# Kernel tuning notes

Hardware: AMD Instinct MI355X
Metric: run time of the kernel (lower is better)

The kernel has to match this reference:

```python
import math
import jax, jax.numpy as jnp
import numpy as np

K = 16  # self.k from init


def knn(x, x2, k):
    # x: [B, d, P], x2: [B, d, S] -> nearest-neighbor indices [B, k, S]
    # (indices into P, per query column of x2). Matches torch knn: topk of
    # negative squared distance along dim=-2.
    x = jax.lax.stop_gradient(x)
    x2 = jax.lax.stop_gradient(x2)
    inner = -2.0 * jnp.einsum('bdp,bds->bps', x, x2)            # [B, P, S]
    xx = jnp.sum(x * x, axis=1)[:, :, None]                      # [B, P, 1]
    xx2 = jnp.sum(x2 * x2, axis=1)[:, None, :]                   # [B, 1, S]
    pd = -xx - inner - xx2                                       # [B, P, S]
    # top-k over the P axis -> move P to last axis for lax.top_k
    _, idx = jax.lax.top_k(jnp.transpose(pd, (0, 2, 1)), k)     # [B, S, k]
    return jnp.transpose(idx, (0, 2, 1))                         # [B, k, S]


def gather_neighbour(X, idx):
    # X: [B, C, P], idx: [B, n, p] -> [B, p, n, C]
    g = jax.vmap(lambda Xb, ib: Xb[:, ib])(X, idx)               # [B, C, n, p]
    return jnp.transpose(g, (0, 3, 2, 1))


def _forward(x, s_num):
    B, C, P = x.shape
    assert s_num <= P
    length = math.ceil(math.sqrt(s_num))                         # 64
    L2 = length * length                                         # == s_num (perfect square)
    mesh = jnp.arange(length, dtype=x.dtype) / length
    m01 = jnp.tile(mesh[None, :], (length, 1)).reshape(1, 1, L2)
    m02 = jnp.tile(mesh[:, None], (1, length)).reshape(1, 1, L2)
    mesh2 = jnp.concatenate([m01, m02], axis=1)                  # [1, 2, L2]
    mesh2 = jnp.broadcast_to(mesh2, (B, 2, L2))

    point_x = x[:, :2, :]                                        # [B, 2, P]
    min_x = jnp.min(point_x, axis=2, keepdims=True)
    max_x = jnp.max(point_x, axis=2, keepdims=True)
    point_sample = mesh2 * (max_x - min_x) + min_x               # [B, 2, L2]

    idx1 = knn(point_x, point_sample, 1)                         # [B, 1, L2]
    sel = gather_neighbour(x, idx1)                              # [B, L2, 1, C]
    select_point = jnp.transpose(sel[:, :, 0, :], (0, 2, 1))     # [B, C, L2]

    idx2 = knn(x[:, :3, :], select_point[:, :3, :], K)           # [B, K, s_num]
    feature = gather_neighbour(x, idx2)                          # [B, s_num, K, C]
    return jnp.transpose(feature, (0, 3, 1, 2))                  # [B, C, s_num, K]


def setup_inputs() -> dict:
    key = jax.random.key(0)
    x = jax.random.normal(key, (8, 5, 16384), dtype=jnp.float32)
    return {"x": x, "s_num": 4096}


def reference(x, s_num):
    return _forward(x, s_num)
```

## Files before the change

kernel.cpp:

```cpp
#include <hip/hip_runtime.h>

#define P 16384
#define S 4096
#define NB 8
#define CAP 16

typedef unsigned long long u64;
typedef unsigned int u32;

#define OPAQUE(x) __asm__("" : "+v"(x))

__device__ __forceinline__ u32 pd_to_dk(float pd) {
  pd = pd + 0.0f;
  u32 b = __float_as_uint(pd);
  u32 s = (u32)((int)b >> 31);
  return b ^ (~(s | 0x80000000u));
}
__device__ __forceinline__ float dk_to_pd(u32 d) {
  u32 pb = (d & 0x80000000u) ? d : (d ^ 0x7FFFFFFFu);
  return __uint_as_float(pb);
}
__device__ __forceinline__ float prev2(float v) {
  u32 b = __float_as_uint(v);
  if ((b & 0x7F800000u) == 0x7F800000u) return v;
  if (v > 0.0f) b -= 2;
  else if (v < 0.0f) b += 2;
  else return -1e-30f;
  return __uint_as_float(b);
}

__device__ __forceinline__ void insert16(u64 (&L)[16], u64 key) {
#pragma unroll
  for (int j = 15; j >= 1; --j) {
    u64 a = (L[j - 1] > key) ? L[j - 1] : key;
    L[j] = (L[j] > key) ? a : L[j];
  }
  L[0] = (L[0] > key) ? key : L[0];
}

__global__ void kminmax(const float* __restrict__ x, float* __restrict__ mm) {
  int b = blockIdx.x;
  int tid = threadIdx.x;
  const float* x0 = x + (size_t)b * 5 * P;
  const float* x1 = x0 + P;
  float mn0 = __builtin_inff(), mx0 = -__builtin_inff();
  float mn1 = __builtin_inff(), mx1 = -__builtin_inff();
  for (int i = tid; i < P; i += 256) {
    float a = x0[i];
    mn0 = fminf(mn0, a); mx0 = fmaxf(mx0, a);
    float c = x1[i];
    mn1 = fminf(mn1, c); mx1 = fmaxf(mx1, c);
  }
  __shared__ float s0[256], s1[256], s2[256], s3[256];
  s0[tid] = mn0; s1[tid] = mx0; s2[tid] = mn1; s3[tid] = mx1;
  __syncthreads();
  for (int off = 128; off > 0; off >>= 1) {
    if (tid < off) {
      s0[tid] = fminf(s0[tid], s0[tid + off]);
      s1[tid] = fmaxf(s1[tid], s1[tid + off]);
      s2[tid] = fminf(s2[tid], s2[tid + off]);
      s3[tid] = fmaxf(s3[tid], s3[tid + off]);
    }
    __syncthreads();
  }
  if (tid == 0) {
    mm[b * 4 + 0] = s0[0];
    mm[b * 4 + 1] = s1[0];
    mm[b * 4 + 2] = s2[0];
    mm[b * 4 + 3] = s3[0];
  }
}

__global__ void kprep(const float* __restrict__ x, float* __restrict__ xx2d,
                      float* __restrict__ xx3d) {
#pragma clang fp contract(off)
  int gid = blockIdx.x * 256 + threadIdx.x;
  int b = gid >> 14;
  int i = gid & (P - 1);
  const float* xs = x + (size_t)b * 5 * P;
  float x0 = xs[i], x1 = xs[P + i], x2 = xs[2 * P + i];
  float t0 = x0 * x0; OPAQUE(t0);
  float t1 = x1 * x1; OPAQUE(t1);
  float t2 = x2 * x2; OPAQUE(t2);
  float s2 = t0 + t1;
  xx2d[gid] = s2;
  xx3d[gid] = s2 + t2;
}

__global__ __launch_bounds__(256) void kidx1(const float* __restrict__ x,
                                             const float* __restrict__ mm,
                                             const float* __restrict__ xx2d,
                                             u64* __restrict__ bests1) {
#pragma clang fp contract(off)
  int blk = blockIdx.x;
  int b = blk >> 8;
  int sgrp = (blk >> 2) & 63;
  int qtr = blk & 3;
  int w = threadIdx.x >> 6, l = threadIdx.x & 63;
  const float* xs = x + (size_t)b * 5 * P;
  const float* ys = xs + P;
  float mn0 = mm[b * 4 + 0], mx0 = mm[b * 4 + 1];
  float mn1 = mm[b * 4 + 2], mx1 = mm[b * 4 + 3];
  float m0 = (float)l * (1.0f / 64.0f);
  float m1 = (float)sgrp * (1.0f / 64.0f);
  float d0 = mx0 - mn0, d1 = mx1 - mn1;
  float p0 = m0 * d0; OPAQUE(p0);
  float q0 = p0 + mn0;
  float p1 = m1 * d1; OPAQUE(p1);
  float q1 = p1 + mn1;
  float sq0 = q0 * q0; OPAQUE(sq0);
  float sq1 = q1 * q1; OPAQUE(sq1);
  float qq = sq0 + sq1;

  int base = qtr * 4096 + w * 1024;
  const float4* xs4 = (const float4*)(xs + base);
  const float4* ys4 = (const float4*)(ys + base);
  const float4* ws4 = (const float4*)(xx2d + b * P + base);
  float best_pd = -__builtin_inff();
  u32 best_idx = 0;
  for (int j = 0; j < 256; ++j) {
    float4 cx = xs4[j];
    float4 cy = ys4[j];
    float4 cw = ws4[j];
    float cxa[4] = {cx.x, cx.y, cx.z, cx.w};
    float cya[4] = {cy.x, cy.y, cy.z, cy.w};
    float cwa[4] = {cw.x, cw.y, cw.z, cw.w};
#pragma unroll
    for (int t = 0; t < 4; ++t) {
      float ip = __builtin_fmaf(cya[t], q1, cxa[t] * q0);
      float a  = __builtin_fmaf(2.0f, ip, -cwa[t]);
      float pd = a - qq;
      bool bt = pd > best_pd;
      best_pd  = bt ? pd : best_pd;
      best_idx = bt ? (u32)(base + (j << 2) + t) : best_idx;
    }
  }
  u64 key = ((u64)pd_to_dk(best_pd) << 32) | best_idx;
  __shared__ u64 kb[4][64];
  kb[w][l] = key;
  __syncthreads();
  if (threadIdx.x < 64) {
    u64 m = kb[0][l];
    u64 t1 = kb[1][l]; m = (t1 < m) ? t1 : m;
    u64 t2 = kb[2][l]; m = (t2 < m) ? t2 : m;
    u64 t3 = kb[3][l]; m = (t3 < m) ? t3 : m;
    bests1[((size_t)((b * 64 + sgrp) * 4 + qtr) << 6) + l] = m;
  }
}

__global__ void kq(const float* __restrict__ x, const u64* __restrict__ bests1,
                   float* __restrict__ qx, float* __restrict__ qy,
                   float* __restrict__ qz) {
  int qi = blockIdx.x * 256 + threadIdx.x;
  int b = qi >> 12;
  int s = qi & 4095;
  int sgrp = s >> 6, l = s & 63;
  size_t o = ((size_t)((b * 64 + sgrp) * 4) << 6) + l;
  u64 m = bests1[o];
  u64 t;
  t = bests1[o + 64];  m = (t < m) ? t : m;
  t = bests1[o + 128]; m = (t < m) ? t : m;
  t = bests1[o + 192]; m = (t < m) ? t : m;
  u32 idx = (u32)m;
  const float* xs = x + (size_t)b * 5 * P;
  qx[qi] = xs[idx];
  qy[qi] = xs[P + idx];
  qz[qi] = xs[2 * P + idx];
}

__global__ __launch_bounds__(512) void kidx2(const float* __restrict__ x,
                                             const float* __restrict__ xx3d,
                                             const float* __restrict__ qx,
                                             const float* __restrict__ qy,
                                             const float* __restrict__ qz,
                                             float* __restrict__ out) {
#pragma clang fp contract(off)
  __shared__ u64 buf[512][CAP + 1];
  __shared__ u64 mgf[64][17];
  int b = blockIdx.x >> 6, sgrp = blockIdx.x & 63;
  int w = threadIdx.x >> 6, l = threadIdx.x & 63;
  int s = (sgrp << 6) + l;
  int qi = (b << 12) + s;
  float q0 = qx[qi], q1 = qy[qi], q2 = qz[qi];
  float sq0 = q0 * q0; OPAQUE(sq0);
  float sq1 = q1 * q1; OPAQUE(sq1);
  float sq2 = q2 * q2; OPAQUE(sq2);
  float qq = (sq0 + sq1) + sq2;
  const float* xs = x + (size_t)b * 5 * P;
  const float* ys = xs + P;
  const float* zs = xs + 2 * P;
  int base = w * 2048;
  const float4* xs4 = (const float4*)(xs + base);
  const float4* ys4 = (const float4*)(ys + base);
  const float4* zs4 = (const float4*)(zs + base);
  const float4* ws4 = (const float4*)(xx3d + b * P + base);

  u64 L[16];
#pragma unroll
  for (int k = 0; k < 16; ++k) L[k] = 0xFF800000FFFFFFFFull;
  float thrA = -__builtin_inff();
  int cnt = 0;
  u64* bufp = buf[threadIdx.x];

  auto drain = [&]() {
    while (__any(cnt > 0)) {
      if (cnt > 0) {
        --cnt;
        u64 e = bufp[cnt];
        float pd = __uint_as_float((u32)(e >> 32)) - qq;
        u64 key = ((u64)pd_to_dk(pd) << 32) | (u32)e;
        if (key < L[15]) insert16(L, key);
      }
    }
    float tp = dk_to_pd((u32)(L[15] >> 32));
    thrA = prev2(tp + qq);
  };

  for (int j = 0; j < 512; ++j) {
    float4 cx = xs4[j];
    float4 cy = ys4[j];
    float4 cz = zs4[j];
    float4 cw = ws4[j];
    float cxa[4] = {cx.x, cx.y, cx.z, cx.w};
    float cya[4] = {cy.x, cy.y, cy.z, cy.w};
    float cza[4] = {cz.x, cz.y, cz.z, cz.w};
    float cwa[4] = {cw.x, cw.y, cw.z, cw.w};
#pragma unroll
    for (int t = 0; t < 4; ++t) {
      float ip = __builtin_fmaf(cza[t], q2,
                                __builtin_fmaf(cya[t], q1, cxa[t] * q0));
      float a  = __builtin_fmaf(2.0f, ip, -cwa[t]);
      if (a >= thrA) {
        bufp[cnt] = ((u64)__float_as_uint(a) << 32) | (u32)(base + (j << 2) + t);
        ++cnt;
      }
    }
    if (__any(cnt >= CAP - 4)) drain();
  }
  drain();

#pragma unroll
  for (int k = 0; k < 16; ++k) bufp[k] = L[k];
  __syncthreads();

  if (w == 0) {
    int p0 = 0, p1 = 0, p2 = 0, p3 = 0, p4 = 0, p5 = 0, p6 = 0, p7 = 0;
    u64 h0 = buf[l][0],        h1 = buf[64 + l][0];
    u64 h2 = buf[128 + l][0],  h3 = buf[192 + l][0];
    u64 h4 = buf[256 + l][0],  h5 = buf[320 + l][0];
    u64 h6 = buf[384 + l][0],  h7 = buf[448 + l][0];
#define ADV(i) { ++p##i; h##i = (p##i < 16) ? buf[i * 64 + l][p##i] : ~0ULL; }
    for (int k = 0; k < 16; ++k) {
      u64 m01 = (h0 < h1) ? h0 : h1;
      u64 m23 = (h2 < h3) ? h2 : h3;
      u64 m45 = (h4 < h5) ? h4 : h5;
      u64 m67 = (h6 < h7) ? h6 : h7;
      u64 ma = (m01 < m23) ? m01 : m23;
      u64 mb = (m45 < m67) ? m45 : m67;
      u64 m = (ma < mb) ? ma : mb;
      mgf[l][k] = m;
      if      (m == h0) ADV(0)
      else if (m == h1) ADV(1)
      else if (m == h2) ADV(2)
      else if (m == h3) ADV(3)
      else if (m == h4) ADV(4)
      else if (m == h5) ADV(5)
      else if (m == h6) ADV(6)
      else              ADV(7)
    }
#undef ADV
  }
  __syncthreads();

  int qrow = threadIdx.x >> 3;
  int g = threadIdx.x & 7;
  int sOut = (sgrp << 6) + qrow;
  u32 i0 = (u32)mgf[qrow][g * 2 + 0];
  u32 i1 = (u32)mgf[qrow][g * 2 + 1];
#pragma unroll
  for (int c = 0; c < 5; ++c) {
    const float* xc = x + (size_t)(b * 5 + c) * P;
    float2 v;
    v.x = xc[i0]; v.y = xc[i1];
    float* op = out + (((size_t)(b * 5 + c) * S + sOut) << 4) + (g << 1);
    *(float2*)op = v;
  }
}

extern "C" void kernel_launch(void* const* d_in, const int* in_sizes, int n_in,
                              void* d_out, int out_size, void* d_ws, size_t ws_size,
                              hipStream_t stream) {
  const float* x = (const float*)d_in[0];
  float* out = (float*)d_out;
  char* ws = (char*)d_ws;
  float* mm    = (float*)ws;
  float* xx2d  = (float*)(ws + 1024);
  float* xx3d  = (float*)(ws + 1024 + 524288);
  u64*   bests1= (u64*)  (ws + 1024 + 2 * 524288);
  float* qx    = (float*)(ws + 1024 + 2 * 524288 + 1048576);
  float* qy    = qx + NB * S;
  float* qz    = qy + NB * S;

  kminmax<<<NB, 256, 0, stream>>>(x, mm);
  kprep<<<NB * P / 256, 256, 0, stream>>>(x, xx2d, xx3d);
  kidx1<<<NB * 256, 256, 0, stream>>>(x, mm, xx2d, bests1);
  kq<<<NB * S / 256, 256, 0, stream>>>(x, bests1, qx, qy, qz);
  kidx2<<<NB * 64, 512, 0, stream>>>(x, xx3d, qx, qy, qz, out);
}
```

Measured before the change: 621.5 us.

## Pack point coords into float4 AoS and split kNN scans across more blocks

```diff
diff --git a/kernel.cpp b/kernel.cpp
--- a/kernel.cpp
+++ b/kernel.cpp
@@ -3,7 +3,7 @@
 #define P 16384
 #define S 4096
 #define NB 8
-#define CAP 16
+#define CAP 8
 
 typedef unsigned long long u64;
 typedef unsigned int u32;
@@ -36,6 +36,15 @@
     L[j] = (L[j] > key) ? a : L[j];
   }
   L[0] = (L[0] > key) ? key : L[0];
+}
+
+__device__ __forceinline__ u64 key3(const float4* __restrict__ pk3b, u32 idx,
+                                    float q0, float q1, float q2, float qq) {
+  float4 v = pk3b[idx];
+  float ip = __builtin_fmaf(v.z, q2, __builtin_fmaf(v.y, q1, v.x * q0));
+  float a  = __builtin_fmaf(2.0f, ip, -v.w);
+  float pd = a - qq;
+  return ((u64)pd_to_dk(pd) << 32) | idx;
 }
 
 __global__ void kminmax(const float* __restrict__ x, float* __restrict__ mm) {
@@ -71,8 +80,8 @@
   }
 }
 
-__global__ void kprep(const float* __restrict__ x, float* __restrict__ xx2d,
-                      float* __restrict__ xx3d) {
+__global__ void kprep(const float* __restrict__ x, float4* __restrict__ pk2,
+                      float4* __restrict__ pk3) {
 #pragma clang fp contract(off)
   int gid = blockIdx.x * 256 + threadIdx.x;
   int b = gid >> 14;
@@ -83,22 +92,19 @@
   float t1 = x1 * x1; OPAQUE(t1);
   float t2 = x2 * x2; OPAQUE(t2);
   float s2 = t0 + t1;
-  xx2d[gid] = s2;
-  xx3d[gid] = s2 + t2;
-}
-
-__global__ __launch_bounds__(256) void kidx1(const float* __restrict__ x,
+  pk2[gid] = make_float4(x0, x1, s2, 0.0f);
+  pk3[gid] = make_float4(x0, x1, x2, s2 + t2);
+}
+
+__global__ __launch_bounds__(256) void kidx1(const float4* __restrict__ pk2,
                                              const float* __restrict__ mm,
-                                             const float* __restrict__ xx2d,
                                              u64* __restrict__ bests1) {
 #pragma clang fp contract(off)
   int blk = blockIdx.x;
-  int b = blk >> 8;
-  int sgrp = (blk >> 2) & 63;
-  int qtr = blk & 3;
+  int b = blk >> 9;
+  int sgrp = (blk >> 3) & 63;
+  int eighth = blk & 7;
   int w = threadIdx.x >> 6, l = threadIdx.x & 63;
-  const float* xs = x + (size_t)b * 5 * P;
-  const float* ys = xs + P;
   float mn0 = mm[b * 4 + 0], mx0 = mm[b * 4 + 1];
   float mn1 = mm[b * 4 + 2], mx1 = mm[b * 4 + 3];
   float m0 = (float)l * (1.0f / 64.0f);
@@ -112,23 +118,16 @@
   float sq1 = q1 * q1; OPAQUE(sq1);
   float qq = sq0 + sq1;
 
-  int base = qtr * 4096 + w * 1024;
-  const float4* xs4 = (const float4*)(xs + base);
-  const float4* ys4 = (const float4*)(ys + base);
-  const float4* ws4 = (const float4*)(xx2d + b * P + base);
+  int base = eighth * 2048 + w * 512;
+  const float4* pc = pk2 + (size_t)b * P + base;
   float best_pd = -__builtin_inff();
   u32 best_idx = 0;
-  for (int j = 0; j < 256; ++j) {
-    float4 cx = xs4[j];
-    float4 cy = ys4[j];
-    float4 cw = ws4[j];
-    float cxa[4] = {cx.x, cx.y, cx.z, cx.w};
-    float cya[4] = {cy.x, cy.y, cy.z, cy.w};
-    float cwa[4] = {cw.x, cw.y, cw.z, cw.w};
+  for (int j = 0; j < 128; ++j) {
 #pragma unroll
     for (int t = 0; t < 4; ++t) {
-      float ip = __builtin_fmaf(cya[t], q1, cxa[t] * q0);
-      float a  = __builtin_fmaf(2.0f, ip, -cwa[t]);
+      float4 v = pc[(j << 2) + t];
+      float ip = __builtin_fmaf(v.y, q1, v.x * q0);
+      float a  = __builtin_fmaf(2.0f, ip, -v.z);
       float pd = a - qq;
       bool bt = pd > best_pd;
       best_pd  = bt ? pd : best_pd;
@@ -144,7 +143,7 @@
     u64 t1 = kb[1][l]; m = (t1 < m) ? t1 : m;
     u64 t2 = kb[2][l]; m = (t2 < m) ? t2 : m;
     u64 t3 = kb[3][l]; m = (t3 < m) ? t3 : m;
-    bests1[((size_t)((b * 64 + sgrp) * 4 + qtr) << 6) + l] = m;
+    bests1[((size_t)((b * 64 + sgrp) * 8 + eighth) << 6) + l] = m;
   }
 }
 
@@ -155,12 +154,13 @@
   int b = qi >> 12;
   int s = qi & 4095;
   int sgrp = s >> 6, l = s & 63;
-  size_t o = ((size_t)((b * 64 + sgrp) * 4) << 6) + l;
+  size_t o = ((size_t)((b * 64 + sgrp) * 8) << 6) + l;
   u64 m = bests1[o];
-  u64 t;
-  t = bests1[o + 64];  m = (t < m) ? t : m;
-  t = bests1[o + 128]; m = (t < m) ? t : m;
-  t = bests1[o + 192]; m = (t < m) ? t : m;
+#pragma unroll
+  for (int i = 1; i < 8; ++i) {
+    u64 t = bests1[o + (size_t)i * 64];
+    m = (t < m) ? t : m;
+  }
   u32 idx = (u32)m;
   const float* xs = x + (size_t)b * 5 * P;
   qx[qi] = xs[idx];
@@ -168,39 +168,35 @@
   qz[qi] = xs[2 * P + idx];
 }
 
-__global__ __launch_bounds__(512) void kidx2(const float* __restrict__ x,
-                                             const float* __restrict__ xx3d,
-                                             const float* __restrict__ qx,
-                                             const float* __restrict__ qy,
-                                             const float* __restrict__ qz,
-                                             float* __restrict__ out) {
+__global__ __launch_bounds__(256, 6) void kidx2(const float4* __restrict__ pk3,
+                                                const float* __restrict__ qx,
+                                                const float* __restrict__ qy,
+                                                const float* __restrict__ qz,
+                                                u32* __restrict__ partial) {
 #pragma clang fp contract(off)
-  __shared__ u64 buf[512][CAP + 1];
-  __shared__ u64 mgf[64][17];
-  int b = blockIdx.x >> 6, sgrp = blockIdx.x & 63;
+  __shared__ u64 buf[256 * (CAP + 1)];
+  u32* stage = (u32*)buf;
+  int blk = blockIdx.x;
+  int b = blk >> 7;
+  int rest = blk & 127;
+  int sgrp = rest >> 1, half = rest & 1;
   int w = threadIdx.x >> 6, l = threadIdx.x & 63;
-  int s = (sgrp << 6) + l;
-  int qi = (b << 12) + s;
+  int qi = (b << 12) + (sgrp << 6) + l;
   float q0 = qx[qi], q1 = qy[qi], q2 = qz[qi];
   float sq0 = q0 * q0; OPAQUE(sq0);
   float sq1 = q1 * q1; OPAQUE(sq1);
   float sq2 = q2 * q2; OPAQUE(sq2);
   float qq = (sq0 + sq1) + sq2;
-  const float* xs = x + (size_t)b * 5 * P;
-  const float* ys = xs + P;
-  const float* zs = xs + 2 * P;
-  int base = w * 2048;
-  const float4* xs4 = (const float4*)(xs + base);
-  const float4* ys4 = (const float4*)(ys + base);
-  const float4* zs4 = (const float4*)(zs + base);
-  const float4* ws4 = (const float4*)(xx3d + b * P + base);
+  const float4* pk3b = pk3 + (size_t)b * P;
+  int base = half * 8192 + w * 2048;
+  const float4* pc = pk3b + base;
 
   u64 L[16];
 #pragma unroll
   for (int k = 0; k < 16; ++k) L[k] = 0xFF800000FFFFFFFFull;
   float thrA = -__builtin_inff();
   int cnt = 0;
-  u64* bufp = buf[threadIdx.x];
+  u64* bufp = buf + threadIdx.x * (CAP + 1);
 
   auto drain = [&]() {
     while (__any(cnt > 0)) {
@@ -217,19 +213,11 @@
   };
 
   for (int j = 0; j < 512; ++j) {
-    float4 cx = xs4[j];
-    float4 cy = ys4[j];
-    float4 cz = zs4[j];
-    float4 cw = ws4[j];
-    float cxa[4] = {cx.x, cx.y, cx.z, cx.w};
-    float cya[4] = {cy.x, cy.y, cy.z, cy.w};
-    float cza[4] = {cz.x, cz.y, cz.z, cz.w};
-    float cwa[4] = {cw.x, cw.y, cw.z, cw.w};
 #pragma unroll
     for (int t = 0; t < 4; ++t) {
-      float ip = __builtin_fmaf(cza[t], q2,
-                                __builtin_fmaf(cya[t], q1, cxa[t] * q0));
-      float a  = __builtin_fmaf(2.0f, ip, -cwa[t]);
+      float4 v = pc[(j << 2) + t];
+      float ip = __builtin_fmaf(v.z, q2, __builtin_fmaf(v.y, q1, v.x * q0));
+      float a  = __builtin_fmaf(2.0f, ip, -v.w);
       if (a >= thrA) {
         bufp[cnt] = ((u64)__float_as_uint(a) << 32) | (u32)(base + (j << 2) + t);
         ++cnt;
@@ -239,51 +227,97 @@
   }
   drain();
 
-#pragma unroll
-  for (int k = 0; k < 16; ++k) bufp[k] = L[k];
-  __syncthreads();
-
-  if (w == 0) {
-    int p0 = 0, p1 = 0, p2 = 0, p3 = 0, p4 = 0, p5 = 0, p6 = 0, p7 = 0;
-    u64 h0 = buf[l][0],        h1 = buf[64 + l][0];
-    u64 h2 = buf[128 + l][0],  h3 = buf[192 + l][0];
-    u64 h4 = buf[256 + l][0],  h5 = buf[320 + l][0];
-    u64 h6 = buf[384 + l][0],  h7 = buf[448 + l][0];
-#define ADV(i) { ++p##i; h##i = (p##i < 16) ? buf[i * 64 + l][p##i] : ~0ULL; }
+  __syncthreads();
+#pragma unroll
+  for (int k = 0; k < 16; ++k) stage[(w << 10) + (l << 4) + k] = (u32)L[k];
+  __syncthreads();
+
+  if ((w & 1) == 0) {
+    const u32* sa = stage + (w << 10) + (l << 4);
+    const u32* sb = stage + ((w + 1) << 10) + (l << 4);
+    int pa = 0, pb = 0;
+    u32 ia = sa[0]; u64 ka = key3(pk3b, ia, q0, q1, q2, qq);
+    u32 ib = sb[0]; u64 kb2 = key3(pk3b, ib, q0, q1, q2, qq);
+    u32* outp = partial + ((((size_t)qi * 2 + half) * 2 + (w >> 1)) << 4);
+    for (int k = 0; k < 16; ++k) {
+      bool ta = ka < kb2;
+      outp[k] = ta ? ia : ib;
+      if (ta) {
+        ++pa;
+        if (pa < 16) { ia = sa[pa]; ka = key3(pk3b, ia, q0, q1, q2, qq); }
+        else ka = ~0ULL;
+      } else {
+        ++pb;
+        if (pb < 16) { ib = sb[pb]; kb2 = key3(pk3b, ib, q0, q1, q2, qq); }
+        else kb2 = ~0ULL;
+      }
+    }
+  }
+}
+
+__global__ __launch_bounds__(256) void km(const float* __restrict__ x,
+                                          const float4* __restrict__ pk3,
+                                          const float* __restrict__ qx,
+                                          const float* __restrict__ qy,
+                                          const float* __restrict__ qz,
+                                          const u32* __restrict__ partial,
+                                          float* __restrict__ out) {
+#pragma clang fp contract(off)
+  __shared__ u32 mg[256][16];
+  int tid = threadIdx.x;
+  int qi0 = blockIdx.x * 256;
+  {
+    int qi = qi0 + tid;
+    int b = qi >> 12;
+    float q0 = qx[qi], q1 = qy[qi], q2 = qz[qi];
+    float sq0 = q0 * q0; OPAQUE(sq0);
+    float sq1 = q1 * q1; OPAQUE(sq1);
+    float sq2 = q2 * q2; OPAQUE(sq2);
+    float qq = (sq0 + sq1) + sq2;
+    const float4* pk3b = pk3 + (size_t)b * P;
+    const u32* lp = partial + ((size_t)qi << 6);
+    int p0 = 0, p1 = 0, p2 = 0, p3 = 0;
+    u32 i0 = lp[0],  i1 = lp[16], i2 = lp[32], i3 = lp[48];
+    u64 h0 = key3(pk3b, i0, q0, q1, q2, qq);
+    u64 h1 = key3(pk3b, i1, q0, q1, q2, qq);
+    u64 h2 = key3(pk3b, i2, q0, q1, q2, qq);
+    u64 h3 = key3(pk3b, i3, q0, q1, q2, qq);
+#define ADVK(n, off) { ++p##n; \
+    if (p##n < 16) { i##n = lp[(off) + p##n]; \
+      h##n = key3(pk3b, i##n, q0, q1, q2, qq); } else h##n = ~0ULL; }
     for (int k = 0; k < 16; ++k) {
       u64 m01 = (h0 < h1) ? h0 : h1;
       u64 m23 = (h2 < h3) ? h2 : h3;
-      u64 m45 = (h4 < h5) ? h4 : h5;
-      u64 m67 = (h6 < h7) ? h6 : h7;
-      u64 ma = (m01 < m23) ? m01 : m23;
-      u64 mb = (m45 < m67) ? m45 : m67;
-      u64 m = (ma < mb) ? ma : mb;
-      mgf[l][k] = m;
-      if      (m == h0) ADV(0)
-      else if (m == h1) ADV(1)
-      else if (m == h2) ADV(2)
-      else if (m == h3) ADV(3)
-      else if (m == h4) ADV(4)
-      else if (m == h5) ADV(5)
-      else if (m == h6) ADV(6)
-      else              ADV(7)
-    }
-#undef ADV
-  }
-  __syncthreads();
-
-  int qrow = threadIdx.x >> 3;
-  int g = threadIdx.x & 7;
-  int sOut = (sgrp << 6) + qrow;
-  u32 i0 = (u32)mgf[qrow][g * 2 + 0];
-  u32 i1 = (u32)mgf[qrow][g * 2 + 1];
-#pragma unroll
-  for (int c = 0; c < 5; ++c) {
-    const float* xc = x + (size_t)(b * 5 + c) * P;
-    float2 v;
-    v.x = xc[i0]; v.y = xc[i1];
-    float* op = out + (((size_t)(b * 5 + c) * S + sOut) << 4) + (g << 1);
-    *(float2*)op = v;
+      u64 m = (m01 < m23) ? m01 : m23;
+      mg[tid][k] = (u32)((m == h0) ? i0 : (m == h1) ? i1 : (m == h2) ? i2 : i3);
+      if      (m == h0) ADVK(0, 0)
+      else if (m == h1) ADVK(1, 16)
+      else if (m == h2) ADVK(2, 32)
+      else              ADVK(3, 48)
+    }
+#undef ADVK
+  }
+  __syncthreads();
+
+#pragma unroll
+  for (int pass = 0; pass < 4; ++pass) {
+    int lq = pass * 64 + (tid >> 2);
+    int g = tid & 3;
+    int qi = qi0 + lq;
+    int b = qi >> 12;
+    int s = qi & 4095;
+    u32 j0 = mg[lq][g * 4 + 0];
+    u32 j1 = mg[lq][g * 4 + 1];
+    u32 j2 = mg[lq][g * 4 + 2];
+    u32 j3 = mg[lq][g * 4 + 3];
+#pragma unroll
+    for (int c = 0; c < 5; ++c) {
+      const float* xc = x + (size_t)(b * 5 + c) * P;
+      float4 v;
+      v.x = xc[j0]; v.y = xc[j1]; v.z = xc[j2]; v.w = xc[j3];
+      float* op = out + (((size_t)(b * 5 + c) * S + s) << 4) + (g << 2);
+      *(float4*)op = v;
+    }
   }
 }
 
@@ -293,17 +327,20 @@
   const float* x = (const float*)d_in[0];
   float* out = (float*)d_out;
   char* ws = (char*)d_ws;
-  float* mm    = (float*)ws;
-  float* xx2d  = (float*)(ws + 1024);
-  float* xx3d  = (float*)(ws + 1024 + 524288);
-  u64*   bests1= (u64*)  (ws + 1024 + 2 * 524288);
-  float* qx    = (float*)(ws + 1024 + 2 * 524288 + 1048576);
-  float* qy    = qx + NB * S;
-  float* qz    = qy + NB * S;
+  size_t off = 0;
+  float*  mm     = (float*)(ws + off);  off += 1024;
+  float4* pk2    = (float4*)(ws + off); off += (size_t)NB * P * 16;
+  float4* pk3    = (float4*)(ws + off); off += (size_t)NB * P * 16;
+  u64*    bests1 = (u64*)(ws + off);    off += (size_t)NB * 64 * 8 * 64 * 8;
+  float*  qx     = (float*)(ws + off);  off += (size_t)NB * S * 4;
+  float*  qy     = (float*)(ws + off);  off += (size_t)NB * S * 4;
+  float*  qz     = (float*)(ws + off);  off += (size_t)NB * S * 4;
+  u32*    partial= (u32*)(ws + off);    off += (size_t)NB * S * 4 * 16 * 4;
 
   kminmax<<<NB, 256, 0, stream>>>(x, mm);
-  kprep<<<NB * P / 256, 256, 0, stream>>>(x, xx2d, xx3d);
-  kidx1<<<NB * 256, 256, 0, stream>>>(x, mm, xx2d, bests1);
+  kprep<<<NB * P / 256, 256, 0, stream>>>(x, pk2, pk3);
+  kidx1<<<NB * 64 * 8, 256, 0, stream>>>(pk2, mm, bests1);
   kq<<<NB * S / 256, 256, 0, stream>>>(x, bests1, qx, qy, qz);
-  kidx2<<<NB * 64, 512, 0, stream>>>(x, xx3d, qx, qy, qz, out);
-}
+  kidx2<<<NB * 64 * 2, 256, 0, stream>>>(pk3, qx, qy, qz, partial);
+  km<<<NB * S / 256, 256, 0, stream>>>(x, pk3, qx, qy, qz, partial, out);
+}
```

After: 867.8 us. +39.6%, slower.

## Split kNN top-16 into value-only threshold pass and index-recovery second pass

Applied to the files above, without the earlier changes.

```diff
diff --git a/kernel.cpp b/kernel.cpp
--- a/kernel.cpp
+++ b/kernel.cpp
@@ -3,7 +3,6 @@
 #define P 16384
 #define S 4096
 #define NB 8
-#define CAP 16
 
 typedef unsigned long long u64;
 typedef unsigned int u32;
@@ -29,10 +28,10 @@
   return __uint_as_float(b);
 }
 
-__device__ __forceinline__ void insert16(u64 (&L)[16], u64 key) {
+__device__ __forceinline__ void insert16u32(u32 (&L)[16], u32 key) {
 #pragma unroll
   for (int j = 15; j >= 1; --j) {
-    u64 a = (L[j - 1] > key) ? L[j - 1] : key;
+    u32 a = (L[j - 1] > key) ? L[j - 1] : key;
     L[j] = (L[j] > key) ? a : L[j];
   }
   L[0] = (L[0] > key) ? key : L[0];
@@ -175,12 +174,12 @@
                                              const float* __restrict__ qz,
                                              float* __restrict__ out) {
 #pragma clang fp contract(off)
-  __shared__ u64 buf[512][CAP + 1];
+  __shared__ u64 smem[512 * 17];
   __shared__ u64 mgf[64][17];
+  const int tid = threadIdx.x;
   int b = blockIdx.x >> 6, sgrp = blockIdx.x & 63;
-  int w = threadIdx.x >> 6, l = threadIdx.x & 63;
-  int s = (sgrp << 6) + l;
-  int qi = (b << 12) + s;
+  int w = tid >> 6, l = tid & 63;
+  int qi = (b << 12) + (sgrp << 6) + l;
   float q0 = qx[qi], q1 = qy[qi], q2 = qz[qi];
   float sq0 = q0 * q0; OPAQUE(sq0);
   float sq1 = q1 * q1; OPAQUE(sq1);
@@ -195,24 +194,24 @@
   const float4* zs4 = (const float4*)(zs + base);
   const float4* ws4 = (const float4*)(xx3d + b * P + base);
 
-  u64 L[16];
-#pragma unroll
-  for (int k = 0; k < 16; ++k) L[k] = 0xFF800000FFFFFFFFull;
+  u32 L[16];
+#pragma unroll
+  for (int k = 0; k < 16; ++k) L[k] = 0xFF800000u;
   float thrA = -__builtin_inff();
   int cnt = 0;
-  u64* bufp = buf[threadIdx.x];
-
-  auto drain = [&]() {
+  u32* arow = (u32*)smem + tid * 13;
+
+  auto drainA = [&]() {
     while (__any(cnt > 0)) {
       if (cnt > 0) {
         --cnt;
-        u64 e = bufp[cnt];
-        float pd = __uint_as_float((u32)(e >> 32)) - qq;
-        u64 key = ((u64)pd_to_dk(pd) << 32) | (u32)e;
-        if (key < L[15]) insert16(L, key);
+        float av = __uint_as_float(arow[cnt]);
+        float pd = av - qq;
+        u32 dk = pd_to_dk(pd);
+        if (dk < L[15]) insert16u32(L, dk);
       }
     }
-    float tp = dk_to_pd((u32)(L[15] >> 32));
+    float tp = dk_to_pd(L[15]);
     thrA = prev2(tp + qq);
   };
 
@@ -230,26 +229,82 @@
       float ip = __builtin_fmaf(cza[t], q2,
                                 __builtin_fmaf(cya[t], q1, cxa[t] * q0));
       float a  = __builtin_fmaf(2.0f, ip, -cwa[t]);
-      if (a >= thrA) {
-        bufp[cnt] = ((u64)__float_as_uint(a) << 32) | (u32)(base + (j << 2) + t);
-        ++cnt;
+      if (a >= thrA) { arow[cnt] = __float_as_uint(a); ++cnt; }
+    }
+    if (__any(cnt >= 8)) drainA();
+  }
+  drainA();
+
+  u32 T = L[15];
+  int c_lt = 0;
+#pragma unroll
+  for (int k = 0; k < 15; ++k) c_lt += (L[k] < T) ? 1 : 0;
+  int need = 16 - c_lt;
+  float T_pd = dk_to_pd(T);
+
+  __syncthreads();
+
+  u64* srow = smem + (size_t)tid * 17;
+  int pc2 = 0, eqc = 0;
+  for (int j = 0; j < 512; ++j) {
+    float4 cx = xs4[j];
+    float4 cy = ys4[j];
+    float4 cz = zs4[j];
+    float4 cw = ws4[j];
+    float cxa[4] = {cx.x, cx.y, cx.z, cx.w};
+    float cya[4] = {cy.x, cy.y, cy.z, cy.w};
+    float cza[4] = {cz.x, cz.y, cz.z, cz.w};
+    float cwa[4] = {cw.x, cw.y, cw.z, cw.w};
+#pragma unroll
+    for (int t = 0; t < 4; ++t) {
+      float ip = __builtin_fmaf(cza[t], q2,
+                                __builtin_fmaf(cya[t], q1, cxa[t] * q0));
+      float a  = __builtin_fmaf(2.0f, ip, -cwa[t]);
+      float pd = a - qq;
+      bool lt = pd > T_pd;
+      bool eq = (pd == T_pd) && (eqc < need);
+      if ((lt || eq) && pc2 < 16) {
+        u32 dk = pd_to_dk(pd);
+        srow[pc2] = ((u64)dk << 32) | (u32)(base + (j << 2) + t);
+        ++pc2;
+        eqc += eq ? 1 : 0;
       }
     }
-    if (__any(cnt >= CAP - 4)) drain();
-  }
-  drain();
-
-#pragma unroll
-  for (int k = 0; k < 16; ++k) bufp[k] = L[k];
+  }
+
+  u64 K[16];
+#pragma unroll
+  for (int k = 0; k < 16; ++k) K[k] = srow[k];
+#pragma unroll
+  for (int p = 1; p < 16; p <<= 1) {
+#pragma unroll
+    for (int k = p; k >= 1; k >>= 1) {
+#pragma unroll
+      for (int j = k & (p - 1); j + k < 16; j += 2 * k) {
+#pragma unroll
+        for (int i = 0; i < k; ++i) {
+          int aa = i + j, bb = i + j + k;
+          if (bb < 16 && (aa / (2 * p)) == (bb / (2 * p))) {
+            u64 xa = K[aa], xb = K[bb];
+            bool g = xa > xb;
+            K[aa] = g ? xb : xa;
+            K[bb] = g ? xa : xb;
+          }
+        }
+      }
+    }
+  }
+#pragma unroll
+  for (int k = 0; k < 16; ++k) srow[k] = K[k];
   __syncthreads();
 
   if (w == 0) {
     int p0 = 0, p1 = 0, p2 = 0, p3 = 0, p4 = 0, p5 = 0, p6 = 0, p7 = 0;
-    u64 h0 = buf[l][0],        h1 = buf[64 + l][0];
-    u64 h2 = buf[128 + l][0],  h3 = buf[192 + l][0];
-    u64 h4 = buf[256 + l][0],  h5 = buf[320 + l][0];
-    u64 h6 = buf[384 + l][0],  h7 = buf[448 + l][0];
-#define ADV(i) { ++p##i; h##i = (p##i < 16) ? buf[i * 64 + l][p##i] : ~0ULL; }
+    u64 h0 = smem[(size_t)(0 * 64 + l) * 17], h1 = smem[(size_t)(1 * 64 + l) * 17];
+    u64 h2 = smem[(size_t)(2 * 64 + l) * 17], h3 = smem[(size_t)(3 * 64 + l) * 17];
+    u64 h4 = smem[(size_t)(4 * 64 + l) * 17], h5 = smem[(size_t)(5 * 64 + l) * 17];
+    u64 h6 = smem[(size_t)(6 * 64 + l) * 17], h7 = smem[(size_t)(7 * 64 + l) * 17];
+#define ADV(i) { ++p##i; h##i = (p##i < 16) ? smem[(size_t)(i * 64 + l) * 17 + p##i] : ~0ULL; }
     for (int k = 0; k < 16; ++k) {
       u64 m01 = (h0 < h1) ? h0 : h1;
       u64 m23 = (h2 < h3) ? h2 : h3;
@@ -272,8 +327,8 @@
   }
   __syncthreads();
 
-  int qrow = threadIdx.x >> 3;
-  int g = threadIdx.x & 7;
+  int qrow = tid >> 3;
+  int g = tid & 7;
   int sOut = (sgrp << 6) + qrow;
   u32 i0 = (u32)mgf[qrow][g * 2 + 0];
   u32 i1 = (u32)mgf[qrow][g * 2 + 1];
```

Measured after the change: 782.2 us. 1.26x slower.

## Pack candidate coordinates and norms into float4 AoS and software-pipeline the scan loops

Applied to the files above, without the earlier changes.

```diff
diff --git a/kernel.cpp b/kernel.cpp
--- a/kernel.cpp
+++ b/kernel.cpp
@@ -71,8 +71,8 @@
   }
 }
 
-__global__ void kprep(const float* __restrict__ x, float* __restrict__ xx2d,
-                      float* __restrict__ xx3d) {
+__global__ void kprep(const float* __restrict__ x, float4* __restrict__ pk2,
+                      float4* __restrict__ pk3) {
 #pragma clang fp contract(off)
   int gid = blockIdx.x * 256 + threadIdx.x;
   int b = gid >> 14;
@@ -83,13 +83,12 @@
   float t1 = x1 * x1; OPAQUE(t1);
   float t2 = x2 * x2; OPAQUE(t2);
   float s2 = t0 + t1;
-  xx2d[gid] = s2;
-  xx3d[gid] = s2 + t2;
-}
-
-__global__ __launch_bounds__(256) void kidx1(const float* __restrict__ x,
+  pk2[gid] = make_float4(x0, x1, s2, 0.0f);
+  pk3[gid] = make_float4(x0, x1, x2, s2 + t2);
+}
+
+__global__ __launch_bounds__(256) void kidx1(const float4* __restrict__ pk2,
                                              const float* __restrict__ mm,
-                                             const float* __restrict__ xx2d,
                                              u64* __restrict__ bests1) {
 #pragma clang fp contract(off)
   int blk = blockIdx.x;
@@ -97,8 +96,6 @@
   int sgrp = (blk >> 2) & 63;
   int qtr = blk & 3;
   int w = threadIdx.x >> 6, l = threadIdx.x & 63;
-  const float* xs = x + (size_t)b * 5 * P;
-  const float* ys = xs + P;
   float mn0 = mm[b * 4 + 0], mx0 = mm[b * 4 + 1];
   float mn1 = mm[b * 4 + 2], mx1 = mm[b * 4 + 3];
   float m0 = (float)l * (1.0f / 64.0f);
@@ -113,28 +110,34 @@
   float qq = sq0 + sq1;
 
   int base = qtr * 4096 + w * 1024;
-  const float4* xs4 = (const float4*)(xs + base);
-  const float4* ys4 = (const float4*)(ys + base);
-  const float4* ws4 = (const float4*)(xx2d + b * P + base);
+  const float4* pc = pk2 + (size_t)b * P + base;
   float best_pd = -__builtin_inff();
   u32 best_idx = 0;
-  for (int j = 0; j < 256; ++j) {
-    float4 cx = xs4[j];
-    float4 cy = ys4[j];
-    float4 cw = ws4[j];
-    float cxa[4] = {cx.x, cx.y, cx.z, cx.w};
-    float cya[4] = {cy.x, cy.y, cy.z, cy.w};
-    float cwa[4] = {cw.x, cw.y, cw.z, cw.w};
-#pragma unroll
-    for (int t = 0; t < 4; ++t) {
-      float ip = __builtin_fmaf(cya[t], q1, cxa[t] * q0);
-      float a  = __builtin_fmaf(2.0f, ip, -cwa[t]);
-      float pd = a - qq;
-      bool bt = pd > best_pd;
-      best_pd  = bt ? pd : best_pd;
-      best_idx = bt ? (u32)(base + (j << 2) + t) : best_idx;
-    }
-  }
+
+  float4 B0[4], B1[4], B2[4], B3[4];
+#define LD1(buf, jv) { const float4* _p = pc + ((jv) << 2); \
+  buf[0] = _p[0]; buf[1] = _p[1]; buf[2] = _p[2]; buf[3] = _p[3]; }
+#define EV1(buf, jv) { _Pragma("unroll") \
+  for (int t = 0; t < 4; ++t) { float4 v = buf[t]; \
+    float ip = __builtin_fmaf(v.y, q1, v.x * q0); \
+    float a  = __builtin_fmaf(2.0f, ip, -v.z); \
+    float pd = a - qq; \
+    bool bt = pd > best_pd; \
+    best_pd  = bt ? pd : best_pd; \
+    best_idx = bt ? (u32)(base + ((jv) << 2) + t) : best_idx; } }
+
+  LD1(B0, 0) LD1(B1, 1) LD1(B2, 2) LD1(B3, 3)
+  for (int jj = 0; jj < 64; ++jj) {
+    int j0 = jj << 2;
+    int nb = (jj < 63) ? ((jj + 1) << 2) : j0;
+    EV1(B0, j0)     LD1(B0, nb)
+    EV1(B1, j0 + 1) LD1(B1, nb + 1)
+    EV1(B2, j0 + 2) LD1(B2, nb + 2)
+    EV1(B3, j0 + 3) LD1(B3, nb + 3)
+  }
+#undef LD1
+#undef EV1
+
   u64 key = ((u64)pd_to_dk(best_pd) << 32) | best_idx;
   __shared__ u64 kb[4][64];
   kb[w][l] = key;
@@ -168,8 +171,8 @@
   qz[qi] = xs[2 * P + idx];
 }
 
-__global__ __launch_bounds__(512) void kidx2(const float* __restrict__ x,
-                                             const float* __restrict__ xx3d,
+__global__ __launch_bounds__(512) void kidx2(const float4* __restrict__ pk3,
+                                             const float* __restrict__ x,
                                              const float* __restrict__ qx,
                                              const float* __restrict__ qy,
                                              const float* __restrict__ qz,
@@ -179,21 +182,14 @@
   __shared__ u64 mgf[64][17];
   int b = blockIdx.x >> 6, sgrp = blockIdx.x & 63;
   int w = threadIdx.x >> 6, l = threadIdx.x & 63;
-  int s = (sgrp << 6) + l;
-  int qi = (b << 12) + s;
+  int qi = (b << 12) + (sgrp << 6) + l;
   float q0 = qx[qi], q1 = qy[qi], q2 = qz[qi];
   float sq0 = q0 * q0; OPAQUE(sq0);
   float sq1 = q1 * q1; OPAQUE(sq1);
   float sq2 = q2 * q2; OPAQUE(sq2);
   float qq = (sq0 + sq1) + sq2;
-  const float* xs = x + (size_t)b * 5 * P;
-  const float* ys = xs + P;
-  const float* zs = xs + 2 * P;
   int base = w * 2048;
-  const float4* xs4 = (const float4*)(xs + base);
-  const float4* ys4 = (const float4*)(ys + base);
-  const float4* zs4 = (const float4*)(zs + base);
-  const float4* ws4 = (const float4*)(xx3d + b * P + base);
+  const float4* pc = pk3 + (size_t)b * P + base;
 
   u64 L[16];
 #pragma unroll
@@ -216,27 +212,30 @@
     thrA = prev2(tp + qq);
   };
 
-  for (int j = 0; j < 512; ++j) {
-    float4 cx = xs4[j];
-    float4 cy = ys4[j];
-    float4 cz = zs4[j];
-    float4 cw = ws4[j];
-    float cxa[4] = {cx.x, cx.y, cx.z, cx.w};
-    float cya[4] = {cy.x, cy.y, cy.z, cy.w};
-    float cza[4] = {cz.x, cz.y, cz.z, cz.w};
-    float cwa[4] = {cw.x, cw.y, cw.z, cw.w};
-#pragma unroll
-    for (int t = 0; t < 4; ++t) {
-      float ip = __builtin_fmaf(cza[t], q2,
-                                __builtin_fmaf(cya[t], q1, cxa[t] * q0));
-      float a  = __builtin_fmaf(2.0f, ip, -cwa[t]);
-      if (a >= thrA) {
-        bufp[cnt] = ((u64)__float_as_uint(a) << 32) | (u32)(base + (j << 2) + t);
-        ++cnt;
-      }
-    }
-    if (__any(cnt >= CAP - 4)) drain();
-  }
+  float4 A0[4], A1[4], A2[4], A3[4];
+#define LD2(bufr, jv) { const float4* _p = pc + ((jv) << 2); \
+  bufr[0] = _p[0]; bufr[1] = _p[1]; bufr[2] = _p[2]; bufr[3] = _p[3]; }
+#define EV2(bufr, jv) { _Pragma("unroll") \
+  for (int t = 0; t < 4; ++t) { float4 v = bufr[t]; \
+    float ip = __builtin_fmaf(v.z, q2, __builtin_fmaf(v.y, q1, v.x * q0)); \
+    float a  = __builtin_fmaf(2.0f, ip, -v.w); \
+    if (a >= thrA) { \
+      bufp[cnt] = ((u64)__float_as_uint(a) << 32) | (u32)(base + ((jv) << 2) + t); \
+      ++cnt; \
+    } } \
+  if (__any(cnt >= CAP - 4)) drain(); }
+
+  LD2(A0, 0) LD2(A1, 1) LD2(A2, 2) LD2(A3, 3)
+  for (int jj = 0; jj < 128; ++jj) {
+    int j0 = jj << 2;
+    int nb = (jj < 127) ? ((jj + 1) << 2) : j0;
+    EV2(A0, j0)     LD2(A0, nb)
+    EV2(A1, j0 + 1) LD2(A1, nb + 1)
+    EV2(A2, j0 + 2) LD2(A2, nb + 2)
+    EV2(A3, j0 + 3) LD2(A3, nb + 3)
+  }
+#undef LD2
+#undef EV2
   drain();
 
 #pragma unroll
@@ -293,17 +292,18 @@
   const float* x = (const float*)d_in[0];
   float* out = (float*)d_out;
   char* ws = (char*)d_ws;
-  float* mm    = (float*)ws;
-  float* xx2d  = (float*)(ws + 1024);
-  float* xx3d  = (float*)(ws + 1024 + 524288);
-  u64*   bests1= (u64*)  (ws + 1024 + 2 * 524288);
-  float* qx    = (float*)(ws + 1024 + 2 * 524288 + 1048576);
-  float* qy    = qx + NB * S;
-  float* qz    = qy + NB * S;
+  size_t off = 0;
+  float*  mm     = (float*)(ws + off);  off += 1024;
+  float4* pk2    = (float4*)(ws + off); off += (size_t)NB * P * 16;
+  float4* pk3    = (float4*)(ws + off); off += (size_t)NB * P * 16;
+  u64*    bests1 = (u64*)(ws + off);    off += (size_t)NB * 64 * 4 * 64 * 8;
+  float*  qx     = (float*)(ws + off);  off += (size_t)NB * S * 4;
+  float*  qy     = (float*)(ws + off);  off += (size_t)NB * S * 4;
+  float*  qz     = (float*)(ws + off);  off += (size_t)NB * S * 4;
 
   kminmax<<<NB, 256, 0, stream>>>(x, mm);
-  kprep<<<NB * P / 256, 256, 0, stream>>>(x, xx2d, xx3d);
-  kidx1<<<NB * 256, 256, 0, stream>>>(x, mm, xx2d, bests1);
+  kprep<<<NB * P / 256, 256, 0, stream>>>(x, pk2, pk3);
+  kidx1<<<NB * 256, 256, 0, stream>>>(pk2, mm, bests1);
   kq<<<NB * S / 256, 256, 0, stream>>>(x, bests1, qx, qy, qz);
-  kidx2<<<NB * 64, 512, 0, stream>>>(x, xx3d, qx, qy, qz, out);
-}
+  kidx2<<<NB * 64, 512, 0, stream>>>(pk3, x, qx, qy, qz, out);
+}
```

Measured after the change: 727.3 us. +17.0%, slower.
